# Kernel optimization log

Measured on AMD Instinct MI355X. Metric: run time of the kernel, lower is better.

The kernel has to match this reference:

```python
import jax, jax.numpy as jnp
import numpy as np

N = 50_000
E = 1_600_000
C_IN, C_HID, C_OUT, M = 128, 128, 2, 4


def gcn_norm(edge_index, num_nodes):
    # GCNConv default: add self-loops, symmetric normalization D^-1/2 (A+I) D^-1/2
    src, dst = edge_index[0], edge_index[1]
    loop = jnp.arange(num_nodes, dtype=edge_index.dtype)
    src = jnp.concatenate([src, loop])
    dst = jnp.concatenate([dst, loop])
    deg = jax.ops.segment_sum(jnp.ones_like(dst, dtype=jnp.float32), dst,
                              num_segments=num_nodes)
    dinv = jnp.where(deg > 0, jax.lax.rsqrt(deg), 0.0)
    norm = dinv[src] * dinv[dst]  # [E+N]
    return src, dst, norm


def propagate(h, src, dst, norm, num_nodes):
    # gather -> scale -> scatter-add (the memory-bound core)
    return jax.ops.segment_sum(h[src] * norm[:, None], dst, num_segments=num_nodes)


def setup_inputs() -> dict:
    key = jax.random.key(0)
    k0, k1, k2, k3 = jax.random.split(key, 4)
    x = jax.random.normal(k0, (N, C_IN), dtype=jnp.float32)
    edge_index = jax.random.randint(k1, (2, E), 0, N, dtype=jnp.int32)
    W1 = jax.random.normal(k2, (C_IN, C_HID), dtype=jnp.float32) * (1.0 / np.sqrt(C_IN))
    b1 = jnp.zeros((C_HID,), dtype=jnp.float32)
    W_out = jax.random.normal(k3, (M, C_HID, C_OUT), dtype=jnp.float32) * (1.0 / np.sqrt(C_HID))
    b_out = jnp.zeros((M, C_OUT), dtype=jnp.float32)
    return {"x": x, "edge_index": edge_index, "W1": W1, "b1": b1,
            "W_out": W_out, "b_out": b_out}


def reference(x, edge_index, W1, b1, W_out, b_out):
    n = x.shape[0]
    src, dst, norm = gcn_norm(edge_index, n)
    # hidden GCNConv + ReLU
    h = x @ W1                                  # [N, C_HID]
    h = propagate(h, src, dst, norm, n) + b1    # [N, C_HID]
    h = jax.nn.relu(h)
    # m output GCNConv heads. GCN propagation is linear in features, so
    # A_hat(h W_m) == (A_hat h) W_m: share one graph traversal across heads.
    agg = propagate(h, src, dst, norm, n)       # [N, C_HID]
    out = jnp.einsum('nf,mfo->mno', agg, W_out) + b_out[:, None, :]  # [M, N, C_OUT]
    return out
```

## Files before the change

### kernel.cpp

```cpp
#include <hip/hip_runtime.h>


constexpr int CIN = 128;
constexpr int SSHIFT = 8;
constexpr int NBLKB = 256;
constexpr int CSR_CAP = 10240;

typedef __attribute__((ext_vector_type(8))) short short8v;
typedef __attribute__((ext_vector_type(4))) float float4v;

__device__ inline unsigned pack_bf16x2(float a, float b) {
  unsigned ua = __float_as_uint(a), ub = __float_as_uint(b);
  ua = (ua + 0x7FFFu + ((ua >> 16) & 1u)) >> 16;
  ub = (ub + 0x7FFFu + ((ub >> 16) & 1u)) >> 16;
  return ua | (ub << 16);
}
__device__ inline float bf_lo(unsigned u) { return __uint_as_float(u << 16); }
__device__ inline float bf_hi(unsigned u) { return __uint_as_float(u & 0xFFFF0000u); }
__device__ inline void split1(float v, unsigned short& h, unsigned short& lo) {
  unsigned ua = __float_as_uint(v);
  unsigned hb = (ua + 0x7FFFu + ((ua >> 16) & 1u)) >> 16;
  float fh = __uint_as_float(hb << 16);
  float rl = v - fh;
  unsigned ub = __float_as_uint(rl);
  h = (unsigned short)hb;
  lo = (unsigned short)((ub + 0x7FFFu + ((ub >> 16) & 1u)) >> 16);
}

__global__ __launch_bounds__(256) void histsb_k(const int* __restrict__ dst,
    int* __restrict__ blockhist, int E, int nsb) {
  __shared__ int lh[256];
  int b = blockIdx.x, t = threadIdx.x;
  lh[t] = 0;
  __syncthreads();
  int per = (E + gridDim.x - 1) / gridDim.x;
  int s0 = b * per, s1 = min(E, s0 + per);
  for (int i = s0 + t; i < s1; i += 256) atomicAdd(&lh[dst[i] >> SSHIFT], 1);
  __syncthreads();
  if (t < nsb) blockhist[t * NBLKB + b] = lh[t];
}

__global__ __launch_bounds__(256) void scan_k(const int* __restrict__ v_in,
    int* __restrict__ excl_out, int* __restrict__ btot, int n) {
  __shared__ int wsum[4];
  int t = threadIdx.x, l = t & 63, w = t >> 6;
  int i = blockIdx.x * 256 + t;
  int v = (i < n) ? v_in[i] : 0;
  int orig = v;
  #pragma unroll
  for (int off = 1; off < 64; off <<= 1) {
    int u = __shfl_up(v, off);
    if (l >= off) v += u;
  }
  if (l == 63) wsum[w] = v;
  __syncthreads();
  int add = 0;
  #pragma unroll
  for (int j = 0; j < 4; ++j) if (j < w) add += wsum[j];
  v += add;
  if (i < n) excl_out[i] = v - orig;
  if (t == 255) btot[blockIdx.x] = v;
}

__global__ __launch_bounds__(256) void stageB_k(const int* __restrict__ src,
    const int* __restrict__ dst, const int* __restrict__ soff,
    const int* __restrict__ btot, unsigned* __restrict__ stage, int E, int nsb) {
  __shared__ int loff[256];
  __shared__ int wsum[4];
  int b = blockIdx.x, t = threadIdx.x, l = t & 63, w = t >> 6;
  int bv = (t < nsb) ? btot[t] : 0;
  int vv = bv;
  #pragma unroll
  for (int o = 1; o < 64; o <<= 1) { int u = __shfl_up(vv, o); if (l >= o) vv += u; }
  if (l == 63) wsum[w] = vv;
  __syncthreads();
  int add = 0;
  #pragma unroll
  for (int j = 0; j < 4; ++j) if (j < w) add += wsum[j];
  int bexcl = vv + add - bv;
  if (t < nsb) loff[t] = soff[t * NBLKB + b] + bexcl;
  __syncthreads();
  int per = (E + gridDim.x - 1) / gridDim.x;
  int s0 = b * per, s1 = min(E, s0 + per);
  for (int i = s0 + t; i < s1; i += 256) {
    int d = dst[i], s = src[i];
    int pos = atomicAdd(&loff[d >> SSHIFT], 1);
    stage[pos] = (unsigned)s | ((unsigned)(d & 255) << 17);
  }
}

__global__ __launch_bounds__(256) void csrsb_k(const unsigned* __restrict__ stage,
    const int* __restrict__ btot, int* __restrict__ row_ptr, int* __restrict__ csr,
    float* __restrict__ dinv, int N, int E, int nsb) {
  __shared__ int cnt[256], off[256], cur[256], sboff[256];
  __shared__ unsigned ebuf[CSR_CAP];
  __shared__ int sbuf[CSR_CAP];
  __shared__ int wsum[4];
  int k = blockIdx.x, t = threadIdx.x, l = t & 63, w = t >> 6;
  cnt[t] = 0; cur[t] = 0;
  {
    int bv = (t < nsb) ? btot[t] : 0;
    int vv = bv;
    #pragma unroll
    for (int o = 1; o < 64; o <<= 1) { int u = __shfl_up(vv, o); if (l >= o) vv += u; }
    if (l == 63) wsum[w] = vv;
    __syncthreads();
    int add = 0;
    #pragma unroll
    for (int j = 0; j < 4; ++j) if (j < w) add += wsum[j];
    sboff[t] = vv + add - bv;
  }
  __syncthreads();
  int r0 = sboff[k];
  int r1 = (k + 1 < nsb) ? sboff[k + 1] : E;
  int len = r1 - r0;
  bool fits = len <= CSR_CAP;
  if (fits) {
    for (int i = t; i < len; i += 256) {
      unsigned s = stage[r0 + i];
      ebuf[i] = s;
      atomicAdd(&cnt[s >> 17], 1);
    }
  } else {
    for (int i = r0 + t; i < r1; i += 256) atomicAdd(&cnt[stage[i] >> 17], 1);
  }
  __syncthreads();
  {
    int v = cnt[t], orig = v;
    #pragma unroll
    for (int o = 1; o < 64; o <<= 1) {
      int u = __shfl_up(v, o);
      if (l >= o) v += u;
    }
    if (l == 63) wsum[w] = v;
    __syncthreads();
    int add = 0;
    #pragma unroll
    for (int j = 0; j < 4; ++j) if (j < w) add += wsum[j];
    int excl = v + add - orig;
    off[t] = excl;
    int n = (k << SSHIFT) + t;
    if (n < N) {
      row_ptr[n] = r0 + excl;
      dinv[n] = rsqrtf((float)(orig + 1));
    }
    if (k == nsb - 1 && t == 255) row_ptr[N] = E;
  }
  __syncthreads();
  if (fits) {
    for (int i = t; i < len; i += 256) {
      unsigned s = ebuf[i];
      int dl = s >> 17;
      int pos = off[dl] + atomicAdd(&cur[dl], 1);
      sbuf[pos] = (int)(s & 0x1FFFF);
    }
    __syncthreads();
    for (int i = t; i < len; i += 256) csr[r0 + i] = sbuf[i];
  } else {
    for (int i = r0 + t; i < r1; i += 256) {
      unsigned s = stage[i];
      int dl = s >> 17;
      int pos = r0 + off[dl] + atomicAdd(&cur[dl], 1);
      csr[pos] = (int)(s & 0x1FFFF);
    }
  }
}

__global__ __launch_bounds__(256) void gemm_k(const float* __restrict__ x,
    const float* __restrict__ W, const float* __restrict__ dinv,
    unsigned* __restrict__ gu, int nrows) {
  __shared__ unsigned short Bh[16384];
  __shared__ unsigned short Bl[16384];
  __shared__ unsigned short Ah[4096];
  __shared__ unsigned short Al[4096];
  int t = threadIdx.x, l = t & 63, w = t >> 6;
  for (int idx = t; idx < 16384; idx += 256) {
    int k = idx >> 7, col = idx & 127;
    unsigned short hb, lb;
    split1(W[idx], hb, lb);
    int addr = (((k >> 5) * 8 + (col >> 4)) * 64 +
                (((k >> 3) & 3) * 16 + (col & 15))) * 8 + (k & 7);
    Bh[addr] = hb;
    Bl[addr] = lb;
  }

  int row0 = blockIdx.x * 128;
  int ct0 = w * 2;
  float4v acc[8][2];
  #pragma unroll
  for (int i = 0; i < 8; ++i) { acc[i][0] = (float4v)0.f; acc[i][1] = (float4v)0.f; }
  int arow = l & 15;
  int kg = l >> 4;
  int srow = t >> 1, skh = t & 1;
  int sgrow = min(row0 + srow, nrows - 1);

  for (int ks = 0; ks < 4; ++ks) {
    __syncthreads();
    {
      const float* xp = &x[(size_t)sgrow * CIN + ks * 32 + skh * 16];
      float f[16];
      *(float4*)&f[0]  = *(const float4*)xp;
      *(float4*)&f[4]  = *(const float4*)(xp + 4);
      *(float4*)&f[8]  = *(const float4*)(xp + 8);
      *(float4*)&f[12] = *(const float4*)(xp + 12);
      #pragma unroll
      for (int h = 0; h < 2; ++h) {
        short8v ah_, al_;
        #pragma unroll
        for (int j = 0; j < 8; ++j) {
          unsigned short hb, lb;
          split1(f[h * 8 + j], hb, lb);
          ah_[j] = (short)hb;
          al_[j] = (short)lb;
        }
        int g = skh * 2 + h;
        *(short8v*)&Ah[(g * 128 + srow) * 8] = ah_;
        *(short8v*)&Al[(g * 128 + srow) * 8] = al_;
      }
    }
    __syncthreads();
    short8v bh0 = *(short8v*)&Bh[((ks * 8 + ct0) * 64 + l) * 8];
    short8v bh1 = *(short8v*)&Bh[((ks * 8 + ct0 + 1) * 64 + l) * 8];
    short8v bl0 = *(short8v*)&Bl[((ks * 8 + ct0) * 64 + l) * 8];
    short8v bl1 = *(short8v*)&Bl[((ks * 8 + ct0 + 1) * 64 + l) * 8];
    #pragma unroll
    for (int rt = 0; rt < 8; ++rt) {
      int ar = arow + rt * 16;
      short8v ah = *(short8v*)&Ah[(kg * 128 + ar) * 8];
      short8v al = *(short8v*)&Al[(kg * 128 + ar) * 8];
      acc[rt][0] = __builtin_amdgcn_mfma_f32_16x16x32_bf16(ah, bh0, acc[rt][0], 0, 0, 0);
      acc[rt][1] = __builtin_amdgcn_mfma_f32_16x16x32_bf16(ah, bh1, acc[rt][1], 0, 0, 0);
      acc[rt][0] = __builtin_amdgcn_mfma_f32_16x16x32_bf16(ah, bl0, acc[rt][0], 0, 0, 0);
      acc[rt][1] = __builtin_amdgcn_mfma_f32_16x16x32_bf16(ah, bl1, acc[rt][1], 0, 0, 0);
      acc[rt][0] = __builtin_amdgcn_mfma_f32_16x16x32_bf16(al, bh0, acc[rt][0], 0, 0, 0);
      acc[rt][1] = __builtin_amdgcn_mfma_f32_16x16x32_bf16(al, bh1, acc[rt][1], 0, 0, 0);
    }
  }
  #pragma unroll
  for (int rt = 0; rt < 8; ++rt) {
    #pragma unroll
    for (int r = 0; r < 4; ++r) {
      int row = row0 + rt * 16 + (l >> 4) * 4 + r;
      bool ok = row < nrows;
      float dv = ok ? dinv[row] : 0.f;
      #pragma unroll
      for (int c = 0; c < 2; ++c) {
        float val = acc[rt][c][r] * dv;
        float other = __shfl_xor(val, 1);
        int col = (ct0 + c) * 16 + (l & 15);
        if (ok && !(l & 1)) gu[(size_t)row * 64 + (col >> 1)] = pack_bf16x2(val, other);
      }
    }
  }
}

#define ACC8(U) do { \
  acc[0] += bf_lo((U).x); acc[1] += bf_hi((U).x); \
  acc[2] += bf_lo((U).y); acc[3] += bf_hi((U).y); \
  acc[4] += bf_lo((U).z); acc[5] += bf_hi((U).z); \
  acc[6] += bf_lo((U).w); acc[7] += bf_hi((U).w); } while (0)

__global__ __launch_bounds__(256) void prop1_k(const uint4* __restrict__ g4,
    const int* __restrict__ row_ptr, const int* __restrict__ csr,
    const float* __restrict__ dinv, const float* __restrict__ b1,
    const float* __restrict__ Wout, unsigned* __restrict__ g2w,
    int n_nodes, int n_waves) {
  int l = threadIdx.x & 63;
  int q = l & 15, sub = l >> 4;
  int wid = (blockIdx.x * blockDim.x + threadIdx.x) >> 6;
  float wj0[8], wj1[8], bb[8];
  #pragma unroll
  for (int c = 0; c < 8; ++c) {
    int col = 8 * q + c;
    wj0[c] = Wout[sub * 256 + col * 2];
    wj1[c] = Wout[sub * 256 + col * 2 + 1];
    bb[c] = b1[col];
  }
  for (int n = wid; n < n_nodes; n += n_waves) {
    int start = row_ptr[n], end = row_ptr[n + 1];
    float d = dinv[n];
    float acc[8];
    #pragma unroll
    for (int c = 0; c < 8; ++c) acc[c] = 0.f;
    for (int base = start; base < end; base += 64) {
      int cnt = min(64, end - base);
      int eb = (base + l < end) ? csr[base + l] : 0;
      int i = 0;
      for (; i + 16 <= cnt; i += 16) {
        int s0 = __shfl(eb, i + sub);
        int s1 = __shfl(eb, i + 4 + sub);
        int s2 = __shfl(eb, i + 8 + sub);
        int s3 = __shfl(eb, i + 12 + sub);
        uint4 u0 = g4[s0 * 16 + q];
        uint4 u1 = g4[s1 * 16 + q];
        uint4 u2 = g4[s2 * 16 + q];
        uint4 u3 = g4[s3 * 16 + q];
        ACC8(u0); ACC8(u1); ACC8(u2); ACC8(u3);
      }
      for (; i + 4 <= cnt; i += 4) {
        int s0 = __shfl(eb, i + sub);
        uint4 u0 = g4[s0 * 16 + q];
        ACC8(u0);
      }
      if (i < cnt) {
        int idx = i + sub;
        bool vld = idx < cnt;
        int s0 = __shfl(eb, vld ? idx : i);
        uint4 u0 = g4[s0 * 16 + q];
        if (vld) { ACC8(u0); }
      }
    }
    #pragma unroll
    for (int c = 0; c < 8; ++c) {
      acc[c] += __shfl_xor(acc[c], 16);
      acc[c] += __shfl_xor(acc[c], 32);
    }
    uint4 us = g4[n * 16 + q];
    ACC8(us);
    float p0 = 0.f, p1 = 0.f;
    #pragma unroll
    for (int c = 0; c < 8; ++c) {
      float y = fmaxf(fmaf(acc[c], d, bb[c]), 0.f);
      p0 = fmaf(y, wj0[c], p0);
      p1 = fmaf(y, wj1[c], p1);
    }
    #pragma unroll
    for (int off = 1; off < 16; off <<= 1) {
      p0 += __shfl_xor(p0, off);
      p1 += __shfl_xor(p1, off);
    }
    if (q == 0) g2w[n * 4 + sub] = pack_bf16x2(d * p0, d * p1);
  }
}

__global__ __launch_bounds__(256) void prop2_k(const uint2* __restrict__ g2v,
    const int* __restrict__ row_ptr, const int* __restrict__ csr,
    const float* __restrict__ dinv, const float* __restrict__ bout,
    float* __restrict__ out, int N) {
  int tid = blockIdx.x * 256 + threadIdx.x;
  int n = tid >> 1, hf = tid & 1;
  if (n >= N) return;
  uint2 us = g2v[n * 2 + hf];
  float a0 = bf_lo(us.x), a1 = bf_hi(us.x);
  float a2 = bf_lo(us.y), a3 = bf_hi(us.y);
  int e = row_ptr[n], e1 = row_ptr[n + 1];
  for (; e + 4 <= e1; e += 4) {
    int i0 = csr[e], i1 = csr[e + 1], i2 = csr[e + 2], i3 = csr[e + 3];
    uint2 u0 = g2v[i0 * 2 + hf], u1 = g2v[i1 * 2 + hf];
    uint2 u2 = g2v[i2 * 2 + hf], u3 = g2v[i3 * 2 + hf];
    a0 += (bf_lo(u0.x) + bf_lo(u1.x)) + (bf_lo(u2.x) + bf_lo(u3.x));
    a1 += (bf_hi(u0.x) + bf_hi(u1.x)) + (bf_hi(u2.x) + bf_hi(u3.x));
    a2 += (bf_lo(u0.y) + bf_lo(u1.y)) + (bf_lo(u2.y) + bf_lo(u3.y));
    a3 += (bf_hi(u0.y) + bf_hi(u1.y)) + (bf_hi(u2.y) + bf_hi(u3.y));
  }
  for (; e < e1; ++e) {
    uint2 u = g2v[csr[e] * 2 + hf];
    a0 += bf_lo(u.x); a1 += bf_hi(u.x);
    a2 += bf_lo(u.y); a3 += bf_hi(u.y);
  }
  float d = dinv[n];
  float2 o0 = make_float2(fmaf(d, a0, bout[hf * 4 + 0]), fmaf(d, a1, bout[hf * 4 + 1]));
  float2 o1 = make_float2(fmaf(d, a2, bout[hf * 4 + 2]), fmaf(d, a3, bout[hf * 4 + 3]));
  *(float2*)&out[(size_t)(hf * 2 + 0) * (2 * N) + 2 * n] = o0;
  *(float2*)&out[(size_t)(hf * 2 + 1) * (2 * N) + 2 * n] = o1;
}

extern "C" void kernel_launch(void* const* d_in, const int* in_sizes, int n_in,
                              void* d_out, int out_size, void* d_ws, size_t ws_size,
                              hipStream_t stream) {
  const float* x    = (const float*)d_in[0];
  const int*   ei   = (const int*)d_in[1];
  const float* W1   = (const float*)d_in[2];
  const float* b1   = (const float*)d_in[3];
  const float* Wout = (const float*)d_in[4];
  const float* bout = (const float*)d_in[5];
  float* out = (float*)d_out;

  const int N = in_sizes[0] / CIN;
  const int E = in_sizes[1] / 2;
  const int* srcp = ei;
  const int* dstp = ei + E;
  const int NSB = (N + 255) >> SSHIFT;
  const int NSC = NSB * NBLKB;

  char* ws = (char*)d_ws;
  size_t off = 0;
  auto alloc = [&](size_t bytes) -> void* {
    void* p = ws + off;
    off = (off + bytes + 511) & ~(size_t)511;
    return p;
  };
  unsigned*       gu        = (unsigned*)alloc((size_t)N * 64 * 4);
  unsigned short* g2u       = (unsigned short*)alloc((size_t)N * 8 * 2);
  float*          dinv      = (float*)alloc((size_t)N * 4);
  int*            blockhist = (int*)alloc((size_t)NSC * 4);
  int*            soff      = (int*)alloc((size_t)NSC * 4);
  int*            btot      = (int*)alloc(256 * 4);
  int*            row_ptr   = (int*)alloc((size_t)(N + 1) * 4);
  int*            csr       = (int*)alloc((size_t)E * 4);
  unsigned*       stage     = (unsigned*)alloc((size_t)E * 4);
  (void)ws_size; (void)n_in; (void)out_size;

  histsb_k<<<NBLKB, 256, 0, stream>>>(dstp, blockhist, E, NSB);
  scan_k<<<NSB, 256, 0, stream>>>(blockhist, soff, btot, NSC);
  stageB_k<<<NBLKB, 256, 0, stream>>>(srcp, dstp, soff, btot, stage, E, NSB);
  csrsb_k<<<NSB, 256, 0, stream>>>(stage, btot, row_ptr, csr, dinv, N, E, NSB);

  gemm_k<<<(N + 127) / 128, 256, 0, stream>>>(x, W1, dinv, gu, N);

  const int P1_BLOCKS = 2048;
  prop1_k<<<P1_BLOCKS, 256, 0, stream>>>((const uint4*)gu, row_ptr, csr, dinv, b1,
                                         Wout, (unsigned*)g2u, N, P1_BLOCKS * 4);
  prop2_k<<<(2 * N + 255) / 256, 256, 0, stream>>>((const uint2*)g2u, row_ptr, csr,
                                                   dinv, bout, out, N);
}
```

Baseline: 135.8 us.

## Split hidden features into four column slices for layer-1 propagation

The GEMM output is stored in a slice-major layout of four 32-column slices, each 64 bytes per node. The first propagation kernel now assigns each block to one slice, so a wave gathers 16 edges at a time at 4 lanes per edge. This shrinks the gathered working set per slice so it fits better in L2/MALL. The per-slice partial head projections go to a float buffer, and a new finalize kernel sums them and packs them to bf16. The cost is four passes over the CSR indices, one extra kernel launch and extra partial-buffer traffic.

```diff
diff --git a/kernel.cpp b/kernel.cpp
--- a/kernel.cpp
+++ b/kernel.cpp
@@ -247,8 +247,11 @@
       for (int c = 0; c < 2; ++c) {
         float val = acc[rt][c][r] * dv;
         float other = __shfl_xor(val, 1);
-        int col = (ct0 + c) * 16 + (l & 15);
-        if (ok && !(l & 1)) gu[(size_t)row * 64 + (col >> 1)] = pack_bf16x2(val, other);
+        int ct = ct0 + c;
+        int slice = ct >> 1;
+        if (ok && !(l & 1))
+          gu[((size_t)slice * nrows + row) * 16 + (ct & 1) * 8 + ((l & 15) >> 1)] =
+              pack_bf16x2(val, other);
       }
     }
   }
@@ -260,23 +263,27 @@
   acc[4] += bf_lo((U).z); acc[5] += bf_hi((U).z); \
   acc[6] += bf_lo((U).w); acc[7] += bf_hi((U).w); } while (0)
 
-__global__ __launch_bounds__(256) void prop1_k(const uint4* __restrict__ g4,
+__global__ __launch_bounds__(256) void prop1s4_k(const uint4* __restrict__ g4,
     const int* __restrict__ row_ptr, const int* __restrict__ csr,
     const float* __restrict__ dinv, const float* __restrict__ b1,
-    const float* __restrict__ Wout, unsigned* __restrict__ g2w,
-    int n_nodes, int n_waves) {
-  int l = threadIdx.x & 63;
-  int q = l & 15, sub = l >> 4;
-  int wid = (blockIdx.x * blockDim.x + threadIdx.x) >> 6;
-  float wj0[8], wj1[8], bb[8];
+    const float* __restrict__ Wout, float* __restrict__ g2part,
+    int N, int waves_per_slice) {
+  int slice = blockIdx.x & 3;
+  int chunk = blockIdx.x >> 2;
+  int t = threadIdx.x, l = t & 63, w = t >> 6;
+  int q = l & 3, sub = l >> 2;
+  int j = sub & 7;
+  float bb[8], wj[8];
   #pragma unroll
   for (int c = 0; c < 8; ++c) {
-    int col = 8 * q + c;
-    wj0[c] = Wout[sub * 256 + col * 2];
-    wj1[c] = Wout[sub * 256 + col * 2 + 1];
+    int col = slice * 32 + 8 * q + c;
     bb[c] = b1[col];
-  }
-  for (int n = wid; n < n_nodes; n += n_waves) {
+    wj[c] = Wout[(j >> 1) * 256 + col * 2 + (j & 1)];
+  }
+  const uint4* gb = g4 + (size_t)slice * N * 4 + q;
+  float* gp = g2part + (size_t)slice * N * 8;
+
+  for (int n = chunk * 4 + w; n < N; n += waves_per_slice) {
     int start = row_ptr[n], end = row_ptr[n + 1];
     float d = dinv[n];
     float acc[8];
@@ -286,51 +293,60 @@
       int cnt = min(64, end - base);
       int eb = (base + l < end) ? csr[base + l] : 0;
       int i = 0;
+      for (; i + 32 <= cnt; i += 32) {
+        int s0 = __shfl(eb, i + sub);
+        int s1 = __shfl(eb, i + 16 + sub);
+        uint4 u0 = gb[(size_t)s0 * 4];
+        uint4 u1 = gb[(size_t)s1 * 4];
+        ACC8(u0); ACC8(u1);
+      }
       for (; i + 16 <= cnt; i += 16) {
         int s0 = __shfl(eb, i + sub);
-        int s1 = __shfl(eb, i + 4 + sub);
-        int s2 = __shfl(eb, i + 8 + sub);
-        int s3 = __shfl(eb, i + 12 + sub);
-        uint4 u0 = g4[s0 * 16 + q];
-        uint4 u1 = g4[s1 * 16 + q];
-        uint4 u2 = g4[s2 * 16 + q];
-        uint4 u3 = g4[s3 * 16 + q];
-        ACC8(u0); ACC8(u1); ACC8(u2); ACC8(u3);
-      }
-      for (; i + 4 <= cnt; i += 4) {
-        int s0 = __shfl(eb, i + sub);
-        uint4 u0 = g4[s0 * 16 + q];
+        uint4 u0 = gb[(size_t)s0 * 4];
         ACC8(u0);
       }
       if (i < cnt) {
         int idx = i + sub;
         bool vld = idx < cnt;
         int s0 = __shfl(eb, vld ? idx : i);
-        uint4 u0 = g4[s0 * 16 + q];
+        uint4 u0 = gb[(size_t)s0 * 4];
         if (vld) { ACC8(u0); }
       }
     }
     #pragma unroll
     for (int c = 0; c < 8; ++c) {
+      acc[c] += __shfl_xor(acc[c], 4);
+      acc[c] += __shfl_xor(acc[c], 8);
       acc[c] += __shfl_xor(acc[c], 16);
       acc[c] += __shfl_xor(acc[c], 32);
     }
-    uint4 us = g4[n * 16 + q];
+    uint4 us = gb[(size_t)n * 4];
     ACC8(us);
-    float p0 = 0.f, p1 = 0.f;
+    float p = 0.f;
     #pragma unroll
     for (int c = 0; c < 8; ++c) {
       float y = fmaxf(fmaf(acc[c], d, bb[c]), 0.f);
-      p0 = fmaf(y, wj0[c], p0);
-      p1 = fmaf(y, wj1[c], p1);
-    }
-    #pragma unroll
-    for (int off = 1; off < 16; off <<= 1) {
-      p0 += __shfl_xor(p0, off);
-      p1 += __shfl_xor(p1, off);
-    }
-    if (q == 0) g2w[n * 4 + sub] = pack_bf16x2(d * p0, d * p1);
-  }
+      p = fmaf(y, wj[c], p);
+    }
+    p += __shfl_xor(p, 1);
+    p += __shfl_xor(p, 2);
+    if (l < 32 && (l & 3) == 0) gp[(size_t)n * 8 + j] = p;
+  }
+}
+
+__global__ __launch_bounds__(256) void finalize_k(const float* __restrict__ g2part,
+    const float* __restrict__ dinv, unsigned* __restrict__ g2w, int N) {
+  int tid = blockIdx.x * 256 + threadIdx.x;
+  if (tid >= N * 4) return;
+  int n = tid >> 2, jp = tid & 3;
+  float s0 = 0.f, s1 = 0.f;
+  #pragma unroll
+  for (int s = 0; s < 4; ++s) {
+    const float* p = &g2part[((size_t)s * N + n) * 8 + jp * 2];
+    s0 += p[0]; s1 += p[1];
+  }
+  float d = dinv[n];
+  g2w[n * 4 + jp] = pack_bf16x2(d * s0, d * s1);
 }
 
 __global__ __launch_bounds__(256) void prop2_k(const uint2* __restrict__ g2v,
@@ -391,6 +407,7 @@
     return p;
   };
   unsigned*       gu        = (unsigned*)alloc((size_t)N * 64 * 4);
+  float*          g2part    = (float*)alloc((size_t)4 * N * 8 * 4);
   unsigned short* g2u       = (unsigned short*)alloc((size_t)N * 8 * 2);
   float*          dinv      = (float*)alloc((size_t)N * 4);
   int*            blockhist = (int*)alloc((size_t)NSC * 4);
@@ -409,8 +426,9 @@
   gemm_k<<<(N + 127) / 128, 256, 0, stream>>>(x, W1, dinv, gu, N);
 
   const int P1_BLOCKS = 2048;
-  prop1_k<<<P1_BLOCKS, 256, 0, stream>>>((const uint4*)gu, row_ptr, csr, dinv, b1,
-                                         Wout, (unsigned*)g2u, N, P1_BLOCKS * 4);
+  prop1s4_k<<<P1_BLOCKS, 256, 0, stream>>>((const uint4*)gu, row_ptr, csr, dinv, b1,
+                                           Wout, g2part, N, (P1_BLOCKS / 4) * 4);
+  finalize_k<<<(N * 4 + 255) / 256, 256, 0, stream>>>(g2part, dinv, (unsigned*)g2u, N);
   prop2_k<<<(2 * N + 255) / 256, 256, 0, stream>>>((const uint2*)g2u, row_ptr, csr,
                                                    dinv, bout, out, N);
 }
```

New measurement: 185.4 us. 36.5% more time.

## Fuse CSR build and both propagations into cooperative kernels with grid syncs

Applied to the files above, without the earlier changes.

Replaces the four CSR-construction launches with one cooperative kernel that uses grid-wide syncs between histogram, scan, staging and per-superblock sort. Also merges the two propagation kernels into one cooperative kernel of 1024 blocks that runs prop1, grid-syncs, then runs prop2 with a grid-stride loop. The aim is to cut kernel launch gaps and inter-kernel drain time. The cost is reduced parallelism: the prep phase is limited to 256 blocks, the prop kernel to 1024 blocks, and the fused prep kernel uses about 80KB of LDS. Grid syncs also add their own overhead. If the cooperative launch fails, the code falls back to the original separate launches.

```diff
diff --git a/kernel.cpp b/kernel.cpp
--- a/kernel.cpp
+++ b/kernel.cpp
@@ -1,4 +1,7 @@
 #include <hip/hip_runtime.h>
+#include <hip/hip_cooperative_groups.h>
+
+namespace cg = cooperative_groups;
 
 
 constexpr int CIN = 128;
@@ -162,6 +165,124 @@
       int dl = s >> 17;
       int pos = r0 + off[dl] + atomicAdd(&cur[dl], 1);
       csr[pos] = (int)(s & 0x1FFFF);
+    }
+  }
+}
+
+__global__ __launch_bounds__(256) void prep_coop_k(const int* __restrict__ src,
+    const int* __restrict__ dst, int* __restrict__ blockhist,
+    int* __restrict__ soff, int* __restrict__ btot, unsigned* __restrict__ stage,
+    int* __restrict__ row_ptr, int* __restrict__ csr, float* __restrict__ dinv,
+    int N, int E, int nsb) {
+  __shared__ int s_a[256], s_b[256], s_c[256], s_d[256];
+  __shared__ int wsum[4];
+  __shared__ unsigned s_ebuf[CSR_CAP];
+  __shared__ int s_sbuf[CSR_CAP];
+  cg::grid_group grid = cg::this_grid();
+  int b = blockIdx.x, t = threadIdx.x, l = t & 63, w = t >> 6;
+  int per = (E + gridDim.x - 1) / gridDim.x;
+  int e0 = b * per, e1 = min(E, e0 + per);
+
+  s_a[t] = 0;
+  __syncthreads();
+  for (int i = e0 + t; i < e1; i += 256) atomicAdd(&s_a[dst[i] >> SSHIFT], 1);
+  __syncthreads();
+  if (t < nsb) blockhist[t * NBLKB + b] = s_a[t];
+  __threadfence();
+  grid.sync();
+
+  if (b < nsb) {
+    int v = blockhist[b * NBLKB + t], orig = v;
+    #pragma unroll
+    for (int o = 1; o < 64; o <<= 1) { int u = __shfl_up(v, o); if (l >= o) v += u; }
+    if (l == 63) wsum[w] = v;
+    __syncthreads();
+    int add = 0;
+    #pragma unroll
+    for (int j = 0; j < 4; ++j) if (j < w) add += wsum[j];
+    v += add;
+    soff[b * NBLKB + t] = v - orig;
+    if (t == 255) btot[b] = v;
+  }
+  __threadfence();
+  grid.sync();
+
+  {
+    int bv = (t < nsb) ? btot[t] : 0;
+    int vv = bv;
+    #pragma unroll
+    for (int o = 1; o < 64; o <<= 1) { int u = __shfl_up(vv, o); if (l >= o) vv += u; }
+    if (l == 63) wsum[w] = vv;
+    __syncthreads();
+    int add = 0;
+    #pragma unroll
+    for (int j = 0; j < 4; ++j) if (j < w) add += wsum[j];
+    int bexcl = vv + add - bv;
+    if (t < nsb) s_b[t] = soff[t * NBLKB + b] + bexcl;
+    if (t < nsb) s_d[t] = bexcl;
+  }
+  __syncthreads();
+  for (int i = e0 + t; i < e1; i += 256) {
+    int d = dst[i], s = src[i];
+    int pos = atomicAdd(&s_b[d >> SSHIFT], 1);
+    stage[pos] = (unsigned)s | ((unsigned)(d & 255) << 17);
+  }
+  __threadfence();
+  grid.sync();
+
+  if (b < nsb) {
+    int k = b;
+    s_a[t] = 0; s_c[t] = 0;
+    __syncthreads();
+    int r0 = s_d[k];
+    int r1 = (k + 1 < nsb) ? s_d[k + 1] : E;
+    int len = r1 - r0;
+    bool fits = len <= CSR_CAP;
+    if (fits) {
+      for (int i = t; i < len; i += 256) {
+        unsigned s = stage[r0 + i];
+        s_ebuf[i] = s;
+        atomicAdd(&s_a[s >> 17], 1);
+      }
+    } else {
+      for (int i = r0 + t; i < r1; i += 256) atomicAdd(&s_a[stage[i] >> 17], 1);
+    }
+    __syncthreads();
+    {
+      int v = s_a[t], orig = v;
+      #pragma unroll
+      for (int o = 1; o < 64; o <<= 1) { int u = __shfl_up(v, o); if (l >= o) v += u; }
+      if (l == 63) wsum[w] = v;
+      __syncthreads();
+      int add = 0;
+      #pragma unroll
+      for (int j = 0; j < 4; ++j) if (j < w) add += wsum[j];
+      int excl = v + add - orig;
+      s_b[t] = excl;
+      int n = (k << SSHIFT) + t;
+      if (n < N) {
+        row_ptr[n] = r0 + excl;
+        dinv[n] = rsqrtf((float)(orig + 1));
+      }
+      if (k == nsb - 1 && t == 255) row_ptr[N] = E;
+    }
+    __syncthreads();
+    if (fits) {
+      for (int i = t; i < len; i += 256) {
+        unsigned s = s_ebuf[i];
+        int dl = s >> 17;
+        int pos = s_b[dl] + atomicAdd(&s_c[dl], 1);
+        s_sbuf[pos] = (int)(s & 0x1FFFF);
+      }
+      __syncthreads();
+      for (int i = t; i < len; i += 256) csr[r0 + i] = s_sbuf[i];
+    } else {
+      for (int i = r0 + t; i < r1; i += 256) {
+        unsigned s = stage[i];
+        int dl = s >> 17;
+        int pos = r0 + s_b[dl] + atomicAdd(&s_c[dl], 1);
+        csr[pos] = (int)(s & 0x1FFFF);
+      }
     }
   }
 }
@@ -260,14 +381,12 @@
   acc[4] += bf_lo((U).z); acc[5] += bf_hi((U).z); \
   acc[6] += bf_lo((U).w); acc[7] += bf_hi((U).w); } while (0)
 
-__global__ __launch_bounds__(256) void prop1_k(const uint4* __restrict__ g4,
+__device__ __forceinline__ void prop1_body(const uint4* __restrict__ g4,
     const int* __restrict__ row_ptr, const int* __restrict__ csr,
     const float* __restrict__ dinv, const float* __restrict__ b1,
     const float* __restrict__ Wout, unsigned* __restrict__ g2w,
-    int n_nodes, int n_waves) {
-  int l = threadIdx.x & 63;
+    int n_nodes, int wid, int n_waves, int l) {
   int q = l & 15, sub = l >> 4;
-  int wid = (blockIdx.x * blockDim.x + threadIdx.x) >> 6;
   float wj0[8], wj1[8], bb[8];
   #pragma unroll
   for (int c = 0; c < 8; ++c) {
@@ -333,36 +452,71 @@
   }
 }
 
+__device__ __forceinline__ void prop2_body(const uint2* __restrict__ g2v,
+    const int* __restrict__ row_ptr, const int* __restrict__ csr,
+    const float* __restrict__ dinv, const float* __restrict__ bout,
+    float* __restrict__ out, int N, int tid, int nthreads) {
+  for (int p = tid; p < 2 * N; p += nthreads) {
+    int n = p >> 1, hf = p & 1;
+    uint2 us = g2v[n * 2 + hf];
+    float a0 = bf_lo(us.x), a1 = bf_hi(us.x);
+    float a2 = bf_lo(us.y), a3 = bf_hi(us.y);
+    int e = row_ptr[n], e1 = row_ptr[n + 1];
+    for (; e + 4 <= e1; e += 4) {
+      int i0 = csr[e], i1 = csr[e + 1], i2 = csr[e + 2], i3 = csr[e + 3];
+      uint2 u0 = g2v[i0 * 2 + hf], u1 = g2v[i1 * 2 + hf];
+      uint2 u2 = g2v[i2 * 2 + hf], u3 = g2v[i3 * 2 + hf];
+      a0 += (bf_lo(u0.x) + bf_lo(u1.x)) + (bf_lo(u2.x) + bf_lo(u3.x));
+      a1 += (bf_hi(u0.x) + bf_hi(u1.x)) + (bf_hi(u2.x) + bf_hi(u3.x));
+      a2 += (bf_lo(u0.y) + bf_lo(u1.y)) + (bf_lo(u2.y) + bf_lo(u3.y));
+      a3 += (bf_hi(u0.y) + bf_hi(u1.y)) + (bf_hi(u2.y) + bf_hi(u3.y));
+    }
+    for (; e < e1; ++e) {
+      uint2 u = g2v[csr[e] * 2 + hf];
+      a0 += bf_lo(u.x); a1 += bf_hi(u.x);
+      a2 += bf_lo(u.y); a3 += bf_hi(u.y);
+    }
+    float d = dinv[n];
+    float2 o0 = make_float2(fmaf(d, a0, bout[hf * 4 + 0]), fmaf(d, a1, bout[hf * 4 + 1]));
+    float2 o1 = make_float2(fmaf(d, a2, bout[hf * 4 + 2]), fmaf(d, a3, bout[hf * 4 + 3]));
+    *(float2*)&out[(size_t)(hf * 2 + 0) * (2 * N) + 2 * n] = o0;
+    *(float2*)&out[(size_t)(hf * 2 + 1) * (2 * N) + 2 * n] = o1;
+  }
+}
+
+__global__ __launch_bounds__(256) void prop1_k(const uint4* __restrict__ g4,
+    const int* __restrict__ row_ptr, const int* __restrict__ csr,
+    const float* __restrict__ dinv, const float* __restrict__ b1,
+    const float* __restrict__ Wout, unsigned* __restrict__ g2w,
+    int n_nodes, int n_waves) {
+  int l = threadIdx.x & 63;
+  int wid = (blockIdx.x * blockDim.x + threadIdx.x) >> 6;
+  prop1_body(g4, row_ptr, csr, dinv, b1, Wout, g2w, n_nodes, wid, n_waves, l);
+}
+
 __global__ __launch_bounds__(256) void prop2_k(const uint2* __restrict__ g2v,
     const int* __restrict__ row_ptr, const int* __restrict__ csr,
     const float* __restrict__ dinv, const float* __restrict__ bout,
     float* __restrict__ out, int N) {
   int tid = blockIdx.x * 256 + threadIdx.x;
-  int n = tid >> 1, hf = tid & 1;
-  if (n >= N) return;
-  uint2 us = g2v[n * 2 + hf];
-  float a0 = bf_lo(us.x), a1 = bf_hi(us.x);
-  float a2 = bf_lo(us.y), a3 = bf_hi(us.y);
-  int e = row_ptr[n], e1 = row_ptr[n + 1];
-  for (; e + 4 <= e1; e += 4) {
-    int i0 = csr[e], i1 = csr[e + 1], i2 = csr[e + 2], i3 = csr[e + 3];
-    uint2 u0 = g2v[i0 * 2 + hf], u1 = g2v[i1 * 2 + hf];
-    uint2 u2 = g2v[i2 * 2 + hf], u3 = g2v[i3 * 2 + hf];
-    a0 += (bf_lo(u0.x) + bf_lo(u1.x)) + (bf_lo(u2.x) + bf_lo(u3.x));
-    a1 += (bf_hi(u0.x) + bf_hi(u1.x)) + (bf_hi(u2.x) + bf_hi(u3.x));
-    a2 += (bf_lo(u0.y) + bf_lo(u1.y)) + (bf_lo(u2.y) + bf_lo(u3.y));
-    a3 += (bf_hi(u0.y) + bf_hi(u1.y)) + (bf_hi(u2.y) + bf_hi(u3.y));
-  }
-  for (; e < e1; ++e) {
-    uint2 u = g2v[csr[e] * 2 + hf];
-    a0 += bf_lo(u.x); a1 += bf_hi(u.x);
-    a2 += bf_lo(u.y); a3 += bf_hi(u.y);
-  }
-  float d = dinv[n];
-  float2 o0 = make_float2(fmaf(d, a0, bout[hf * 4 + 0]), fmaf(d, a1, bout[hf * 4 + 1]));
-  float2 o1 = make_float2(fmaf(d, a2, bout[hf * 4 + 2]), fmaf(d, a3, bout[hf * 4 + 3]));
-  *(float2*)&out[(size_t)(hf * 2 + 0) * (2 * N) + 2 * n] = o0;
-  *(float2*)&out[(size_t)(hf * 2 + 1) * (2 * N) + 2 * n] = o1;
+  prop2_body(g2v, row_ptr, csr, dinv, bout, out, N, tid, gridDim.x * 256);
+}
+
+__global__ __launch_bounds__(256, 4) void prop12_coop_k(const uint4* __restrict__ g4,
+    const int* __restrict__ row_ptr, const int* __restrict__ csr,
+    const float* __restrict__ dinv, const float* __restrict__ b1,
+    const float* __restrict__ Wout, unsigned* __restrict__ g2w,
+    const float* __restrict__ bout, float* __restrict__ out, int N) {
+  cg::grid_group grid = cg::this_grid();
+  int l = threadIdx.x & 63;
+  int wid = (blockIdx.x * blockDim.x + threadIdx.x) >> 6;
+  int n_waves = (gridDim.x * blockDim.x) >> 6;
+  prop1_body(g4, row_ptr, csr, dinv, b1, Wout, g2w, N, wid, n_waves, l);
+  __threadfence();
+  grid.sync();
+  int tid = blockIdx.x * 256 + threadIdx.x;
+  prop2_body((const uint2*)g2w, row_ptr, csr, dinv, bout, out, N,
+             tid, gridDim.x * 256);
 }
 
 extern "C" void kernel_launch(void* const* d_in, const int* in_sizes, int n_in,
@@ -401,16 +555,40 @@
   unsigned*       stage     = (unsigned*)alloc((size_t)E * 4);
   (void)ws_size; (void)n_in; (void)out_size;
 
-  histsb_k<<<NBLKB, 256, 0, stream>>>(dstp, blockhist, E, NSB);
-  scan_k<<<NSB, 256, 0, stream>>>(blockhist, soff, btot, NSC);
-  stageB_k<<<NBLKB, 256, 0, stream>>>(srcp, dstp, soff, btot, stage, E, NSB);
-  csrsb_k<<<NSB, 256, 0, stream>>>(stage, btot, row_ptr, csr, dinv, N, E, NSB);
+  {
+    int Nv = N, Ev = E, NSBv = NSB;
+    void* args[] = {(void*)&srcp, (void*)&dstp, (void*)&blockhist, (void*)&soff,
+                    (void*)&btot, (void*)&stage, (void*)&row_ptr, (void*)&csr,
+                    (void*)&dinv, (void*)&Nv, (void*)&Ev, (void*)&NSBv};
+    hipError_t err = hipLaunchCooperativeKernel(
+        reinterpret_cast<void*>(prep_coop_k), dim3(NBLKB), dim3(256), args, 0, stream);
+    if (err != hipSuccess) {
+      (void)hipGetLastError();
+      histsb_k<<<NBLKB, 256, 0, stream>>>(dstp, blockhist, E, NSB);
+      scan_k<<<NSB, 256, 0, stream>>>(blockhist, soff, btot, NSC);
+      stageB_k<<<NBLKB, 256, 0, stream>>>(srcp, dstp, soff, btot, stage, E, NSB);
+      csrsb_k<<<NSB, 256, 0, stream>>>(stage, btot, row_ptr, csr, dinv, N, E, NSB);
+    }
+  }
 
   gemm_k<<<(N + 127) / 128, 256, 0, stream>>>(x, W1, dinv, gu, N);
 
-  const int P1_BLOCKS = 2048;
-  prop1_k<<<P1_BLOCKS, 256, 0, stream>>>((const uint4*)gu, row_ptr, csr, dinv, b1,
-                                         Wout, (unsigned*)g2u, N, P1_BLOCKS * 4);
-  prop2_k<<<(2 * N + 255) / 256, 256, 0, stream>>>((const uint2*)g2u, row_ptr, csr,
-                                                   dinv, bout, out, N);
-}
+  {
+    const uint4* g4p = (const uint4*)gu;
+    unsigned* g2wp = (unsigned*)g2u;
+    int Nv = N;
+    void* args[] = {(void*)&g4p, (void*)&row_ptr, (void*)&csr, (void*)&dinv,
+                    (void*)&b1, (void*)&Wout, (void*)&g2wp, (void*)&bout,
+                    (void*)&out, (void*)&Nv};
+    hipError_t err = hipLaunchCooperativeKernel(
+        reinterpret_cast<void*>(prop12_coop_k), dim3(1024), dim3(256), args, 0, stream);
+    if (err != hipSuccess) {
+      (void)hipGetLastError();
+      const int P1_BLOCKS = 2048;
+      prop1_k<<<P1_BLOCKS, 256, 0, stream>>>(g4p, row_ptr, csr, dinv, b1,
+                                             Wout, g2wp, N, P1_BLOCKS * 4);
+      prop2_k<<<(2 * N + 255) / 256, 256, 0, stream>>>((const uint2*)g2u, row_ptr,
+                                                       csr, dinv, bout, out, N);
+    }
+  }
+}
```

Result: slower. 520.4 us (+283.1%).
